# Performance work log

Hardware: AMD Instinct MI355X
Metric: run time of the kernel (lower is better)

The kernel has to match this reference:

```python
import jax, jax.numpy as jnp
import numpy as np

T, KBLK, EMB, B = 2048, 64, 512, 4


def _make_coords(t, k):
    # head1: for each j, cols = block_start(j) + arange(j % k + 1)  (block-causal local)
    j = np.arange(t)
    cnt1 = (j % k) + 1
    rows1 = np.repeat(j, cnt1)
    off1 = np.arange(cnt1.sum()) - np.repeat(np.cumsum(cnt1) - cnt1, cnt1)
    cols1 = (rows1 // k) * k + off1
    # head2: for each block start c, rows = arange(c, t), col = c  (strided block-start)
    starts = np.arange(t // k) * k
    cnt2 = t - starts
    base = np.repeat(starts, cnt2)
    off2 = np.arange(cnt2.sum()) - np.repeat(np.cumsum(cnt2) - cnt2, cnt2)
    rows2, cols2 = base + off2, base
    c1 = np.stack([rows1, cols1], 1).astype(np.int32)
    c2 = np.stack([rows2, cols2], 1).astype(np.int32)
    return c1, c2


def setup_inputs() -> dict:
    key = jax.random.key(0)
    ks = jax.random.split(key, 6)
    s = 1.0 / float(np.sqrt(EMB))
    c1, c2 = _make_coords(T, KBLK)
    return {
        "x": jax.random.normal(ks[0], (B, T, EMB), jnp.float32),
        "Wk": jax.random.normal(ks[1], (EMB, EMB), jnp.float32) * s,
        "bk": jnp.zeros((EMB,), jnp.float32),
        "Wq": jax.random.normal(ks[2], (EMB, EMB), jnp.float32) * s,
        "bq": jnp.zeros((EMB,), jnp.float32),
        "Wv": jax.random.normal(ks[3], (EMB, EMB), jnp.float32) * s,
        "bv": jnp.zeros((EMB,), jnp.float32),
        "Wu": jax.random.normal(ks[4], (EMB, 2 * EMB), jnp.float32) * s,
        "bu": jnp.zeros((EMB,), jnp.float32),
        "coords1": jnp.asarray(c1),
        "coords2": jnp.asarray(c2),
    }


def _sparse_head(Kt, Qt, Vt, coords):
    rows, cols = coords[:, 0], coords[:, 1]
    # dot[b,p] = (K @ Q^T)[b, rows[p], cols[p]] = K[b,rows[p],:] . Q[b,cols[p],:]
    dot = jnp.einsum('bpe,bpe->bp', Kt[:, rows], Qt[:, cols])
    # sparse.batchmm: out[b,r] = sum_{p: rows[p]=r} dot[b,p] * V[b, cols[p]]
    out = jnp.zeros_like(Vt).at[:, rows].add(dot[..., None] * Vt[:, cols])
    return out


def reference(x, Wk, bk, Wq, bq, Wv, bv, Wu, bu, coords1, coords2):
    Kt = x @ Wk.T + bk
    Qt = x @ Wq.T + bq
    Vt = x @ Wv.T + bv
    h1 = _sparse_head(Kt, Qt, Vt, coords1)
    h2 = _sparse_head(Kt, Qt, Vt, coords2)
    comb = jnp.concatenate([h1, h2], axis=-1)  # [B, T, 2*EMB]
    return comb @ Wu.T + bu
```

## Files before the change

kernel.cpp:

```cpp
#include <hip/hip_runtime.h>


typedef unsigned short u16;
typedef __attribute__((ext_vector_type(8))) short short8;
typedef __attribute__((ext_vector_type(4))) float f32x4;

constexpr int TDIM  = 2048;
constexpr int EMB_D = 512;
constexpr int BB    = 4;
constexpr int NBLK  = 32;
constexpr int LDK   = 2048;

__device__ __forceinline__ u16 f2b(float f) {
    unsigned u = __float_as_uint(f);
    unsigned r = (u + 0x7FFFu + ((u >> 16) & 1u)) >> 16;
    return (u16)r;
}

__global__ __launch_bounds__(256) void prep_k(
    const float* __restrict__ x, const float* __restrict__ Wk, const float* __restrict__ Wq,
    const float* __restrict__ Wv, const float* __restrict__ Wu,
    const float* __restrict__ bk, const float* __restrict__ bq, const float* __restrict__ bv,
    u16* __restrict__ xb, u16* __restrict__ wcat, u16* __restrict__ wvtb,
    u16* __restrict__ wub, float* __restrict__ biascat)
{
    const int bid = blockIdx.x, tid = threadIdx.x;
    if (bid < 5120) {
        const float* src; u16* dst; int base;
        if (bid < 4096)      { src = x;  dst = xb;            base = bid * 1024; }
        else if (bid < 4352) { src = Wk; dst = wcat;          base = (bid - 4096) * 1024; }
        else if (bid < 4608) { src = Wq; dst = wcat + 262144; base = (bid - 4352) * 1024; }
        else                 { src = Wu; dst = wub;           base = (bid - 4608) * 1024; }
        const int idx = base + tid * 4;
        float4 v = *(const float4*)(src + idx);
        ushort4 o = { f2b(v.x), f2b(v.y), f2b(v.z), f2b(v.w) };
        *(ushort4*)(dst + idx) = o;
    } else if (bid < 5184) {
        __shared__ float T[64][65];
        const int t = bid - 5120;
        const int j0 = (t >> 3) * 64, k0 = (t & 7) * 64;
        const int rr = tid >> 4, c4 = (tid & 15) * 4;
        #pragma unroll
        for (int it = 0; it < 4; ++it) {
            const int j = rr + it * 16;
            float4 v = *(const float4*)(Wv + (size_t)(j0 + j) * 512 + k0 + c4);
            T[c4+0][j] = v.x; T[c4+1][j] = v.y; T[c4+2][j] = v.z; T[c4+3][j] = v.w;
        }
        __syncthreads();
        #pragma unroll
        for (int it = 0; it < 4; ++it) {
            const int k = rr + it * 16;
            ushort4 o = { f2b(T[k][c4+0]), f2b(T[k][c4+1]), f2b(T[k][c4+2]), f2b(T[k][c4+3]) };
            *(ushort4*)(wvtb + (size_t)(k0 + k) * 512 + j0 + c4) = o;
        }
    } else if (bid < 5200) {
        const int o = (bid - 5184) * 64 + (tid >> 2);
        const int p = tid & 3;
        const int n = o & 511, half = o >> 9;
        const float* wr = Wu + (size_t)n * 1024 + half * 512 + p * 128;
        const float* br = bv + p * 128;
        float s = 0.f;
        #pragma unroll
        for (int j = 0; j < 128; j += 4) {
            float4 a = *(const float4*)(wr + j);
            float4 b = *(const float4*)(br + j);
            s += a.x*b.x + a.y*b.y + a.z*b.z + a.w*b.w;
        }
        s += __shfl_xor(s, 1);
        s += __shfl_xor(s, 2);
        if (p == 0) biascat[1024 + o] = s;
    } else {
        const int idx = tid * 4;
        float4 v = (idx < 512) ? *(const float4*)(bk + idx)
                               : *(const float4*)(bq + idx - 512);
        *(float4*)(biascat + idx) = v;
    }
}

__global__ __launch_bounds__(256) void wc_gemm_k(
    const u16* __restrict__ wub, const u16* __restrict__ wvtb, u16* __restrict__ wcat)
{
    __shared__ u16 As[128 * 32];
    __shared__ u16 Bs[128 * 32];
    const int bm = blockIdx.x * 128;
    const int bn = blockIdx.y * 128;
    const int tid  = threadIdx.x;
    const int wid  = tid >> 6;
    const int lane = tid & 63;
    const int l15  = lane & 15;
    const int quad = lane >> 4;
    const int wm = (wid & 1) * 64;
    const int wn = (wid >> 1) * 64;

    f32x4 acc[4][4] = {};

    const int srow  = tid >> 2;
    const int skoff = (tid & 3) * 8;
    const int m0 = bm + srow, m1 = bm + 64 + srow;
    const u16* Ag0 = wub + (size_t)(m0 & 511) * 1024 + (m0 >> 9) * 512 + skoff;
    const u16* Ag1 = wub + (size_t)(m1 & 511) * 1024 + (m1 >> 9) * 512 + skoff;
    const u16* Bg  = wvtb + (size_t)(bn + srow) * 512 + skoff;
    char* AsBase = (char*)As + wid * 1024;
    char* BsBase = (char*)Bs + wid * 1024;

    for (int k0 = 0; k0 < 512; k0 += 32) {
        __syncthreads();
        __builtin_amdgcn_global_load_lds(
            (const __attribute__((address_space(1))) void*)(Ag0 + k0),
            (__attribute__((address_space(3))) void*)AsBase, 16, 0, 0);
        __builtin_amdgcn_global_load_lds(
            (const __attribute__((address_space(1))) void*)(Ag1 + k0),
            (__attribute__((address_space(3))) void*)(AsBase + 4096), 16, 0, 0);
        __builtin_amdgcn_global_load_lds(
            (const __attribute__((address_space(1))) void*)(Bg + k0),
            (__attribute__((address_space(3))) void*)BsBase, 16, 0, 0);
        __builtin_amdgcn_global_load_lds(
            (const __attribute__((address_space(1))) void*)(Bg + (size_t)64 * 512 + k0),
            (__attribute__((address_space(3))) void*)(BsBase + 4096), 16, 0, 0);
        __syncthreads();

        short8 a[4], b[4];
        #pragma unroll
        for (int i = 0; i < 4; ++i)
            a[i] = *(const short8*)((const short*)As + (wm + 16 * i + l15) * 32 + quad * 8);
        #pragma unroll
        for (int j = 0; j < 4; ++j)
            b[j] = *(const short8*)((const short*)Bs + (wn + 16 * j + l15) * 32 + quad * 8);
        #pragma unroll
        for (int i = 0; i < 4; ++i)
            #pragma unroll
            for (int j = 0; j < 4; ++j)
                acc[i][j] = __builtin_amdgcn_mfma_f32_16x16x32_bf16(a[i], b[j], acc[i][j], 0, 0, 0);
    }

    #pragma unroll
    for (int i = 0; i < 4; ++i)
        #pragma unroll
        for (int j = 0; j < 4; ++j) {
            const int col = bn + wn + 16 * j + l15;
            #pragma unroll
            for (int r = 0; r < 4; ++r) {
                const int row = bm + wm + 16 * i + quad * 4 + r;
                wcat[(size_t)(1024 + row) * 512 + col] = f2b(acc[i][j][r]);
            }
        }
}

template<int MH, int KK>
__device__ __forceinline__ void mm16(const short8 (&a)[4], const short8 (&b)[2][4],
                                     f32x4 (&acc)[8][4])
{
    #pragma unroll
    for (int f = 0; f < 4; ++f)
        #pragma unroll
        for (int g = 0; g < 4; ++g)
            acc[MH * 4 + f][g] = __builtin_amdgcn_mfma_f32_16x16x32_bf16(
                a[f], b[KK][g], acc[MH * 4 + f][g], 0, 0, 0);
}

template<int SLOT, int MH>
__device__ __forceinline__ void lda4(short8 (&a)[4], const u16* sm, int arow, int koff)
{
    #pragma unroll
    for (int f = 0; f < 4; ++f)
        a[f] = *(const short8*)(sm + SLOT * 32768 + (arow + MH * 64 + f * 16) * 64 + koff);
}

template<int SLOT>
__device__ __forceinline__ void ldb4(short8 (&bk)[4], const u16* sm, int brow, int koff)
{
    #pragma unroll
    for (int g = 0; g < 4; ++g)
        bk[g] = *(const short8*)(sm + SLOT * 32768 + 16384 + (brow + g * 16) * 64 + koff);
}

#define STA(S, CI, T) __builtin_amdgcn_global_load_lds( \
    (const __attribute__((address_space(1))) void*)(Ag + (size_t)(CI) * 32768 + (T) * 64), \
    (__attribute__((address_space(3))) void*)(sm + (S) * 32768 + (CI) * 4096 + wid * 512), 16, 0, 0)
#define STB(S, CI, T) __builtin_amdgcn_global_load_lds( \
    (const __attribute__((address_space(1))) void*)(Bg + (size_t)(CI) * 32768 + (T) * 64), \
    (__attribute__((address_space(3))) void*)(sm + (S) * 32768 + 16384 + (CI) * 4096 + wid * 512), 16, 0, 0)
#define KBAR()  __builtin_amdgcn_s_barrier()
#define KPRIO(P) __builtin_amdgcn_s_setprio(P)
#define LGKM0() do { asm volatile("s_waitcnt lgkmcnt(0)" ::: "memory"); \
                     __builtin_amdgcn_sched_barrier(0); } while (0)
#define VMC4()  asm volatile("s_waitcnt vmcnt(4)" ::: "memory")
#define VMC0()  asm volatile("s_waitcnt vmcnt(0)" ::: "memory")

__global__ __launch_bounds__(512, 2) void kqv_gemm_k(
    const u16* __restrict__ A, const u16* __restrict__ W,
    const float* __restrict__ bias, u16* __restrict__ C)
{
    __shared__ u16 sm[65536];

    const int bid = blockIdx.x;
    const int wg  = (bid & 7) * 32 + (bid >> 3);
    const int bm  = (wg & 31) * 256;
    const int bn  = (wg >> 5) * 256;
    const int tid  = threadIdx.x;
    const int wid  = tid >> 6;
    const int lane = tid & 63;
    const int l15  = lane & 15;
    const int quad = lane >> 4;
    const int wm = wid >> 2;
    const int wn = wid & 3;

    const int stgrow = wid * 8 + (lane >> 3);
    const int stgk   = ((lane & 7) ^ ((lane >> 3) & 7)) << 3;
    const u16* Ag = A + (size_t)(bm + stgrow) * 512 + stgk;
    const u16* Bg = W + (size_t)(bn + stgrow) * 512 + stgk;

    const int r7     = l15 & 7;
    const int arow   = wm * 128 + l15;
    const int brow   = wn * 64 + l15;
    const int off_k0 = ((quad ^ r7) << 3);
    const int off_k1 = (((4 | quad) ^ r7) << 3);

    f32x4 acc[8][4] = {};
    short8 a[4], b[2][4];

    STA(0,0,0); STA(0,2,0); STB(0,0,0); STB(0,1,0);
    STB(0,2,0); STB(0,3,0); STA(0,1,0); STA(0,3,0);
    STA(1,0,1); STA(1,2,1); STB(1,0,1); STB(1,1,1);
    VMC4(); KBAR();

    for (int it = 0; it < 3; ++it) {
        const int t = 2 * it;
        ldb4<0>(b[0], sm, brow, off_k0); lda4<0,0>(a, sm, arow, off_k0);
        STB(1,2,t+1); STB(1,3,t+1);
        KBAR(); LGKM0(); KPRIO(1); mm16<0,0>(a, b, acc); KPRIO(0); KBAR();
        ldb4<0>(b[1], sm, brow, off_k1); lda4<0,0>(a, sm, arow, off_k1);
        STA(1,1,t+1); STA(1,3,t+1);
        KBAR(); LGKM0(); KPRIO(1); mm16<0,1>(a, b, acc); KPRIO(0); KBAR();
        lda4<0,1>(a, sm, arow, off_k0);
        STA(0,0,t+2); STA(0,2,t+2);
        KBAR(); LGKM0(); KPRIO(1); mm16<1,0>(a, b, acc); KPRIO(0); KBAR();
        lda4<0,1>(a, sm, arow, off_k1);
        STB(0,0,t+2); STB(0,1,t+2);
        KBAR(); LGKM0(); KPRIO(1); mm16<1,1>(a, b, acc); KPRIO(0); VMC4(); KBAR();
        ldb4<1>(b[0], sm, brow, off_k0); lda4<1,0>(a, sm, arow, off_k0);
        STB(0,2,t+2); STB(0,3,t+2);
        KBAR(); LGKM0(); KPRIO(1); mm16<0,0>(a, b, acc); KPRIO(0); KBAR();
        ldb4<1>(b[1], sm, brow, off_k1); lda4<1,0>(a, sm, arow, off_k1);
        STA(0,1,t+2); STA(0,3,t+2);
        KBAR(); LGKM0(); KPRIO(1); mm16<0,1>(a, b, acc); KPRIO(0); KBAR();
        lda4<1,1>(a, sm, arow, off_k0);
        STA(1,0,t+3); STA(1,2,t+3);
        KBAR(); LGKM0(); KPRIO(1); mm16<1,0>(a, b, acc); KPRIO(0); KBAR();
        lda4<1,1>(a, sm, arow, off_k1);
        STB(1,0,t+3); STB(1,1,t+3);
        KBAR(); LGKM0(); KPRIO(1); mm16<1,1>(a, b, acc); KPRIO(0); VMC4(); KBAR();
    }

    ldb4<0>(b[0], sm, brow, off_k0); lda4<0,0>(a, sm, arow, off_k0);
    STB(1,2,7); STB(1,3,7);
    KBAR(); LGKM0(); KPRIO(1); mm16<0,0>(a, b, acc); KPRIO(0); KBAR();
    ldb4<0>(b[1], sm, brow, off_k1); lda4<0,0>(a, sm, arow, off_k1);
    STA(1,1,7); STA(1,3,7);
    KBAR(); LGKM0(); KPRIO(1); mm16<0,1>(a, b, acc); KPRIO(0); KBAR();
    lda4<0,1>(a, sm, arow, off_k0);
    KBAR(); LGKM0(); KPRIO(1); mm16<1,0>(a, b, acc); KPRIO(0); KBAR();
    lda4<0,1>(a, sm, arow, off_k1);
    KBAR(); LGKM0(); KPRIO(1); mm16<1,1>(a, b, acc); KPRIO(0); VMC0(); KBAR();
    ldb4<1>(b[0], sm, brow, off_k0); lda4<1,0>(a, sm, arow, off_k0);
    KBAR(); LGKM0(); KPRIO(1); mm16<0,0>(a, b, acc); KPRIO(0); KBAR();
    ldb4<1>(b[1], sm, brow, off_k1); lda4<1,0>(a, sm, arow, off_k1);
    KBAR(); LGKM0(); KPRIO(1); mm16<0,1>(a, b, acc); KPRIO(0); KBAR();
    lda4<1,1>(a, sm, arow, off_k0);
    KBAR(); LGKM0(); KPRIO(1); mm16<1,0>(a, b, acc); KPRIO(0); KBAR();
    lda4<1,1>(a, sm, arow, off_k1);
    KBAR(); LGKM0(); KPRIO(1); mm16<1,1>(a, b, acc); KPRIO(0);

    #pragma unroll
    for (int mf = 0; mf < 8; ++mf) {
        #pragma unroll
        for (int g = 0; g < 4; ++g) {
            const int col = bn + wn * 64 + g * 16 + l15;
            const float bvv = bias[col];
            #pragma unroll
            for (int r = 0; r < 4; ++r) {
                const int row = bm + wm * 128 + mf * 16 + quad * 4 + r;
                C[(size_t)row * LDK + col] = f2b(acc[mf][g][r] + bvv);
            }
        }
    }
}

#undef STA
#undef STB
#undef KBAR
#undef KPRIO
#undef LGKM0
#undef VMC4
#undef VMC0

__global__ __launch_bounds__(256) void heads_k(
    const u16* __restrict__ KQV, const float* __restrict__ bu, float* __restrict__ out)
{
    __shared__ u16 smA[64 * 104];
    __shared__ u16 smVT[128 * 104];
    __shared__ u16 pK[2][64 * 32];
    __shared__ u16 pQ[2][64 * 32];
    __shared__ u16 pQs[2][32 * 32];

    const int blk = blockIdx.x, b = blockIdx.y;
    const int e0 = blockIdx.z * 128;
    const int tid = threadIdx.x;
    const int wid = tid >> 6, lane = tid & 63;
    const int l15 = lane & 15, quad = lane >> 4;
    const size_t row0 = (size_t)b * TDIM + (size_t)blk * 64;
    const size_t brow = (size_t)b * TDIM;
    const int srow_base = 16 * wid + quad * 4;

    #pragma unroll
    for (int it = 0; it < 4; ++it) {
        const int id = tid + 256 * it;
        const int c  = id & 63;
        const int eo = (id >> 6) * 8;
        short8 v = *(const short8*)(KQV + (row0 + c) * (size_t)LDK + 1024 + e0 + eo);
        #pragma unroll
        for (int i = 0; i < 8; ++i) smVT[(eo + i) * 104 + c] = (u16)v[i];
    }
    #pragma unroll
    for (int it = 0; it < 2; ++it) {
        const int id = tid + 256 * it;
        const int m  = id & 31;
        const int eo = (id >> 5) * 8;
        short8 v = *(const short8*)(KQV + (brow + 64 * m) * (size_t)LDK + 1536 + e0 + eo);
        #pragma unroll
        for (int i = 0; i < 8; ++i) smVT[(eo + i) * 104 + 64 + m] = (u16)v[i];
    }

    f32x4 s1[4] = {}; f32x4 s2[2] = {};
    const int srow  = tid >> 2;
    const int skoff = (tid & 3) * 8;
    const int qsrow = srow & 31;
    const int qsp   = tid >> 7;
    const u16* Kg  = KQV + (row0 + srow) * (size_t)LDK + skoff;
    const u16* Qg  = KQV + (row0 + srow) * (size_t)LDK + 512 + skoff;
    const u16* Qsg = KQV + (brow + (size_t)64 * qsrow) * (size_t)LDK + 512 + qsp * 32 + skoff;
    char* dK  = (char*)pK  + wid * 1024;
    char* dQ  = (char*)pQ  + wid * 1024;
    char* dQs = (char*)pQs + wid * 1024;

    for (int k0 = 0; k0 < 512; k0 += 64) {
        __syncthreads();
        __builtin_amdgcn_global_load_lds(
            (const __attribute__((address_space(1))) void*)(Kg + k0),
            (__attribute__((address_space(3))) void*)dK, 16, 0, 0);
        __builtin_amdgcn_global_load_lds(
            (const __attribute__((address_space(1))) void*)(Kg + k0 + 32),
            (__attribute__((address_space(3))) void*)(dK + 4096), 16, 0, 0);
        __builtin_amdgcn_global_load_lds(
            (const __attribute__((address_space(1))) void*)(Qg + k0),
            (__attribute__((address_space(3))) void*)dQ, 16, 0, 0);
        __builtin_amdgcn_global_load_lds(
            (const __attribute__((address_space(1))) void*)(Qg + k0 + 32),
            (__attribute__((address_space(3))) void*)(dQ + 4096), 16, 0, 0);
        __builtin_amdgcn_global_load_lds(
            (const __attribute__((address_space(1))) void*)(Qsg + k0),
            (__attribute__((address_space(3))) void*)dQs, 16, 0, 0);
        __syncthreads();

        short8 a0 = *(const short8*)(pK[0] + (16 * wid + l15) * 32 + quad * 8);
        short8 a1 = *(const short8*)(pK[1] + (16 * wid + l15) * 32 + quad * 8);
        #pragma unroll
        for (int j = 0; j < 4; ++j) {
            short8 b0 = *(const short8*)(pQ[0] + (16 * j + l15) * 32 + quad * 8);
            short8 b1 = *(const short8*)(pQ[1] + (16 * j + l15) * 32 + quad * 8);
            s1[j] = __builtin_amdgcn_mfma_f32_16x16x32_bf16(a0, b0, s1[j], 0, 0, 0);
            s1[j] = __builtin_amdgcn_mfma_f32_16x16x32_bf16(a1, b1, s1[j], 0, 0, 0);
        }
        #pragma unroll
        for (int j = 0; j < 2; ++j) {
            short8 b0 = *(const short8*)(pQs[0] + (16 * j + l15) * 32 + quad * 8);
            short8 b1 = *(const short8*)(pQs[1] + (16 * j + l15) * 32 + quad * 8);
            s2[j] = __builtin_amdgcn_mfma_f32_16x16x32_bf16(a0, b0, s2[j], 0, 0, 0);
            s2[j] = __builtin_amdgcn_mfma_f32_16x16x32_bf16(a1, b1, s2[j], 0, 0, 0);
        }
    }

    #pragma unroll
    for (int j = 0; j < 4; ++j)
        #pragma unroll
        for (int r = 0; r < 4; ++r) {
            const int rr = srow_base + r;
            const int cc = 16 * j + l15;
            smA[rr * 104 + cc] = f2b((cc <= rr) ? s1[j][r] : 0.0f);
        }
    #pragma unroll
    for (int j = 0; j < 2; ++j)
        #pragma unroll
        for (int r = 0; r < 4; ++r) {
            const int m  = 16 * j + l15;
            const int rr = srow_base + r;
            smA[rr * 104 + 64 + m] = f2b((m <= blk) ? s2[j][r] : 0.0f);
        }
    __syncthreads();

    f32x4 o[8] = {};
    const u16* arow = smA + (16 * wid + l15) * 104;
    #pragma unroll
    for (int ks = 0; ks < 3; ++ks) {
        short8 as = *(const short8*)(arow + 32 * ks + quad * 8);
        #pragma unroll
        for (int nt = 0; nt < 8; ++nt) {
            short8 bs = *(const short8*)(smVT + (16 * nt + l15) * 104 + 32 * ks + quad * 8);
            o[nt] = __builtin_amdgcn_mfma_f32_16x16x32_bf16(as, bs, o[nt], 0, 0, 0);
        }
    }
    #pragma unroll
    for (int nt = 0; nt < 8; ++nt) {
        const int col = e0 + 16 * nt + l15;
        const float bvv = bu[col];
        #pragma unroll
        for (int r = 0; r < 4; ++r)
            out[(row0 + srow_base + r) * (size_t)EMB_D + col] = o[nt][r] + bvv;
    }
}

extern "C" void kernel_launch(void* const* d_in, const int* in_sizes, int n_in,
                              void* d_out, int out_size, void* d_ws, size_t ws_size,
                              hipStream_t stream)
{
    const float* x  = (const float*)d_in[0];
    const float* Wk = (const float*)d_in[1];
    const float* bk = (const float*)d_in[2];
    const float* Wq = (const float*)d_in[3];
    const float* bq = (const float*)d_in[4];
    const float* Wv = (const float*)d_in[5];
    const float* bv = (const float*)d_in[6];
    const float* Wu = (const float*)d_in[7];
    const float* bu = (const float*)d_in[8];
    float* out = (float*)d_out;

    char* w = (char*)d_ws;
    u16*   KQV     = (u16*)  (w + ((size_t)0  << 20));
    u16*   xb      = (u16*)  (w + ((size_t)32 << 20));
    u16*   wcat    = (u16*)  (w + ((size_t)40 << 20));
    u16*   wvtb    = (u16*)  (w + ((size_t)42 << 20));
    u16*   wub     = (u16*)  (w + ((size_t)43 << 20));
    float* biascat = (float*)(w + ((size_t)44 << 20));

    hipLaunchKernelGGL(prep_k, dim3(5201), dim3(256), 0, stream,
                       x, Wk, Wq, Wv, Wu, bk, bq, bv, xb, wcat, wvtb, wub, biascat);
    hipLaunchKernelGGL(wc_gemm_k, dim3(8, 4), dim3(256), 0, stream, wub, wvtb, wcat);
    hipLaunchKernelGGL(kqv_gemm_k, dim3(256), dim3(512), 0, stream, xb, wcat, biascat, KQV);
    hipLaunchKernelGGL(heads_k, dim3(NBLK, BB, 4), dim3(256), 0, stream, KQV, bu, out);
}
```

Before: 144.4 us.

## Fuse Wu·Wv weight GEMM into prep kernel and stage KQV stores through LDS

The separate wc_gemm_k launch and the intermediate bf16 copies of Wu and transposed Wv are removed. The first 32 blocks of prep_k now compute the Wu·Wv product directly from fp32 global memory, converting to bf16 in registers, which saves one launch and two intermediate buffers. The Wv operand is read with strided scalar loads, and these 32 long blocks may now sit on the critical path of prep_k. Separately, the KQV GEMM epilogue writes results into shared memory first and then issues coalesced 16-byte row stores, replacing scattered 2-byte global writes.

```diff
diff --git a/kernel.cpp b/kernel.cpp
--- a/kernel.cpp
+++ b/kernel.cpp
@@ -21,40 +21,80 @@
     const float* __restrict__ x, const float* __restrict__ Wk, const float* __restrict__ Wq,
     const float* __restrict__ Wv, const float* __restrict__ Wu,
     const float* __restrict__ bk, const float* __restrict__ bq, const float* __restrict__ bv,
-    u16* __restrict__ xb, u16* __restrict__ wcat, u16* __restrict__ wvtb,
-    u16* __restrict__ wub, float* __restrict__ biascat)
+    u16* __restrict__ xb, u16* __restrict__ wcat, float* __restrict__ biascat)
 {
     const int bid = blockIdx.x, tid = threadIdx.x;
-    if (bid < 5120) {
+    if (bid < 32) {
+        const int bm = (bid >> 2) * 128;
+        const int bn = (bid & 3) * 128;
+        const int wid  = tid >> 6;
+        const int lane = tid & 63;
+        const int l15  = lane & 15;
+        const int quad = lane >> 4;
+        const int wm = (wid & 1) * 64;
+        const int wn = (wid >> 1) * 64;
+
+        f32x4 acc[4][4] = {};
+
+        const float* Arow[4];
+        #pragma unroll
+        for (int i = 0; i < 4; ++i) {
+            const int m = bm + wm + 16 * i + l15;
+            Arow[i] = Wu + (size_t)(m & 511) * 1024 + (m >> 9) * 512 + quad * 8;
+        }
+        const float* Bcol[4];
+        #pragma unroll
+        for (int g = 0; g < 4; ++g)
+            Bcol[g] = Wv + (bn + wn + 16 * g + l15) + (size_t)(quad * 8) * 512;
+
+        for (int j0 = 0; j0 < 512; j0 += 32) {
+            short8 a[4], b[4];
+            #pragma unroll
+            for (int i = 0; i < 4; ++i) {
+                float4 v0 = *(const float4*)(Arow[i] + j0);
+                float4 v1 = *(const float4*)(Arow[i] + j0 + 4);
+                a[i] = (short8){(short)f2b(v0.x), (short)f2b(v0.y), (short)f2b(v0.z), (short)f2b(v0.w),
+                                (short)f2b(v1.x), (short)f2b(v1.y), (short)f2b(v1.z), (short)f2b(v1.w)};
+            }
+            #pragma unroll
+            for (int g = 0; g < 4; ++g) {
+                const float* p = Bcol[g] + (size_t)j0 * 512;
+                float v0 = p[0];          float v1 = p[512];
+                float v2 = p[1024];       float v3 = p[1536];
+                float v4 = p[2048];       float v5 = p[2560];
+                float v6 = p[3072];       float v7 = p[3584];
+                b[g] = (short8){(short)f2b(v0), (short)f2b(v1), (short)f2b(v2), (short)f2b(v3),
+                                (short)f2b(v4), (short)f2b(v5), (short)f2b(v6), (short)f2b(v7)};
+            }
+            #pragma unroll
+            for (int i = 0; i < 4; ++i)
+                #pragma unroll
+                for (int g = 0; g < 4; ++g)
+                    acc[i][g] = __builtin_amdgcn_mfma_f32_16x16x32_bf16(a[i], b[g], acc[i][g], 0, 0, 0);
+        }
+
+        #pragma unroll
+        for (int i = 0; i < 4; ++i)
+            #pragma unroll
+            for (int g = 0; g < 4; ++g) {
+                const int col = bn + wn + 16 * g + l15;
+                #pragma unroll
+                for (int r = 0; r < 4; ++r) {
+                    const int row = bm + wm + 16 * i + quad * 4 + r;
+                    wcat[(size_t)(1024 + row) * 512 + col] = f2b(acc[i][g][r]);
+                }
+            }
+    } else if (bid < 4640) {
         const float* src; u16* dst; int base;
-        if (bid < 4096)      { src = x;  dst = xb;            base = bid * 1024; }
-        else if (bid < 4352) { src = Wk; dst = wcat;          base = (bid - 4096) * 1024; }
-        else if (bid < 4608) { src = Wq; dst = wcat + 262144; base = (bid - 4352) * 1024; }
-        else                 { src = Wu; dst = wub;           base = (bid - 4608) * 1024; }
+        if (bid < 4128)      { src = x;  dst = xb;            base = (bid - 32) * 1024; }
+        else if (bid < 4384) { src = Wk; dst = wcat;          base = (bid - 4128) * 1024; }
+        else                 { src = Wq; dst = wcat + 262144; base = (bid - 4384) * 1024; }
         const int idx = base + tid * 4;
         float4 v = *(const float4*)(src + idx);
         ushort4 o = { f2b(v.x), f2b(v.y), f2b(v.z), f2b(v.w) };
         *(ushort4*)(dst + idx) = o;
-    } else if (bid < 5184) {
-        __shared__ float T[64][65];
-        const int t = bid - 5120;
-        const int j0 = (t >> 3) * 64, k0 = (t & 7) * 64;
-        const int rr = tid >> 4, c4 = (tid & 15) * 4;
-        #pragma unroll
-        for (int it = 0; it < 4; ++it) {
-            const int j = rr + it * 16;
-            float4 v = *(const float4*)(Wv + (size_t)(j0 + j) * 512 + k0 + c4);
-            T[c4+0][j] = v.x; T[c4+1][j] = v.y; T[c4+2][j] = v.z; T[c4+3][j] = v.w;
-        }
-        __syncthreads();
-        #pragma unroll
-        for (int it = 0; it < 4; ++it) {
-            const int k = rr + it * 16;
-            ushort4 o = { f2b(T[k][c4+0]), f2b(T[k][c4+1]), f2b(T[k][c4+2]), f2b(T[k][c4+3]) };
-            *(ushort4*)(wvtb + (size_t)(k0 + k) * 512 + j0 + c4) = o;
-        }
-    } else if (bid < 5200) {
-        const int o = (bid - 5184) * 64 + (tid >> 2);
+    } else if (bid < 4656) {
+        const int o = (bid - 4640) * 64 + (tid >> 2);
         const int p = tid & 3;
         const int n = o & 511, half = o >> 9;
         const float* wr = Wu + (size_t)n * 1024 + half * 512 + p * 128;
@@ -75,75 +115,6 @@
                                : *(const float4*)(bq + idx - 512);
         *(float4*)(biascat + idx) = v;
     }
-}
-
-__global__ __launch_bounds__(256) void wc_gemm_k(
-    const u16* __restrict__ wub, const u16* __restrict__ wvtb, u16* __restrict__ wcat)
-{
-    __shared__ u16 As[128 * 32];
-    __shared__ u16 Bs[128 * 32];
-    const int bm = blockIdx.x * 128;
-    const int bn = blockIdx.y * 128;
-    const int tid  = threadIdx.x;
-    const int wid  = tid >> 6;
-    const int lane = tid & 63;
-    const int l15  = lane & 15;
-    const int quad = lane >> 4;
-    const int wm = (wid & 1) * 64;
-    const int wn = (wid >> 1) * 64;
-
-    f32x4 acc[4][4] = {};
-
-    const int srow  = tid >> 2;
-    const int skoff = (tid & 3) * 8;
-    const int m0 = bm + srow, m1 = bm + 64 + srow;
-    const u16* Ag0 = wub + (size_t)(m0 & 511) * 1024 + (m0 >> 9) * 512 + skoff;
-    const u16* Ag1 = wub + (size_t)(m1 & 511) * 1024 + (m1 >> 9) * 512 + skoff;
-    const u16* Bg  = wvtb + (size_t)(bn + srow) * 512 + skoff;
-    char* AsBase = (char*)As + wid * 1024;
-    char* BsBase = (char*)Bs + wid * 1024;
-
-    for (int k0 = 0; k0 < 512; k0 += 32) {
-        __syncthreads();
-        __builtin_amdgcn_global_load_lds(
-            (const __attribute__((address_space(1))) void*)(Ag0 + k0),
-            (__attribute__((address_space(3))) void*)AsBase, 16, 0, 0);
-        __builtin_amdgcn_global_load_lds(
-            (const __attribute__((address_space(1))) void*)(Ag1 + k0),
-            (__attribute__((address_space(3))) void*)(AsBase + 4096), 16, 0, 0);
-        __builtin_amdgcn_global_load_lds(
-            (const __attribute__((address_space(1))) void*)(Bg + k0),
-            (__attribute__((address_space(3))) void*)BsBase, 16, 0, 0);
-        __builtin_amdgcn_global_load_lds(
-            (const __attribute__((address_space(1))) void*)(Bg + (size_t)64 * 512 + k0),
-            (__attribute__((address_space(3))) void*)(BsBase + 4096), 16, 0, 0);
-        __syncthreads();
-
-        short8 a[4], b[4];
-        #pragma unroll
-        for (int i = 0; i < 4; ++i)
-            a[i] = *(const short8*)((const short*)As + (wm + 16 * i + l15) * 32 + quad * 8);
-        #pragma unroll
-        for (int j = 0; j < 4; ++j)
-            b[j] = *(const short8*)((const short*)Bs + (wn + 16 * j + l15) * 32 + quad * 8);
-        #pragma unroll
-        for (int i = 0; i < 4; ++i)
-            #pragma unroll
-            for (int j = 0; j < 4; ++j)
-                acc[i][j] = __builtin_amdgcn_mfma_f32_16x16x32_bf16(a[i], b[j], acc[i][j], 0, 0, 0);
-    }
-
-    #pragma unroll
-    for (int i = 0; i < 4; ++i)
-        #pragma unroll
-        for (int j = 0; j < 4; ++j) {
-            const int col = bn + wn + 16 * j + l15;
-            #pragma unroll
-            for (int r = 0; r < 4; ++r) {
-                const int row = bm + wm + 16 * i + quad * 4 + r;
-                wcat[(size_t)(1024 + row) * 512 + col] = f2b(acc[i][j][r]);
-            }
-        }
 }
 
 template<int MH, int KK>
@@ -271,17 +242,29 @@
     lda4<1,1>(a, sm, arow, off_k1);
     KBAR(); LGKM0(); KPRIO(1); mm16<1,1>(a, b, acc); KPRIO(0);
 
+    __syncthreads();
     #pragma unroll
     for (int mf = 0; mf < 8; ++mf) {
         #pragma unroll
         for (int g = 0; g < 4; ++g) {
-            const int col = bn + wn * 64 + g * 16 + l15;
-            const float bvv = bias[col];
+            const int col = wn * 64 + g * 16 + l15;
+            const float bvv = bias[bn + col];
             #pragma unroll
             for (int r = 0; r < 4; ++r) {
-                const int row = bm + wm * 128 + mf * 16 + quad * 4 + r;
-                C[(size_t)row * LDK + col] = f2b(acc[mf][g][r] + bvv);
+                const int row = wm * 128 + mf * 16 + quad * 4 + r;
+                sm[row * 256 + col] = f2b(acc[mf][g][r] + bvv);
             }
+        }
+    }
+    __syncthreads();
+    {
+        const int rr = tid >> 5;
+        const int ck = tid & 31;
+        #pragma unroll
+        for (int p = 0; p < 16; ++p) {
+            const int row = p * 16 + rr;
+            short8 v = *(const short8*)(sm + row * 256 + ck * 8);
+            *(short8*)(C + (size_t)(bm + row) * LDK + bn + ck * 8) = v;
         }
     }
 }
@@ -438,13 +421,10 @@
     u16*   KQV     = (u16*)  (w + ((size_t)0  << 20));
     u16*   xb      = (u16*)  (w + ((size_t)32 << 20));
     u16*   wcat    = (u16*)  (w + ((size_t)40 << 20));
-    u16*   wvtb    = (u16*)  (w + ((size_t)42 << 20));
-    u16*   wub     = (u16*)  (w + ((size_t)43 << 20));
     float* biascat = (float*)(w + ((size_t)44 << 20));
 
-    hipLaunchKernelGGL(prep_k, dim3(5201), dim3(256), 0, stream,
-                       x, Wk, Wq, Wv, Wu, bk, bq, bv, xb, wcat, wvtb, wub, biascat);
-    hipLaunchKernelGGL(wc_gemm_k, dim3(8, 4), dim3(256), 0, stream, wub, wvtb, wcat);
+    hipLaunchKernelGGL(prep_k, dim3(4657), dim3(256), 0, stream,
+                       x, Wk, Wq, Wv, Wu, bk, bq, bv, xb, wcat, biascat);
     hipLaunchKernelGGL(kqv_gemm_k, dim3(256), dim3(512), 0, stream, xb, wcat, biascat, KQV);
     hipLaunchKernelGGL(heads_k, dim3(NBLK, BB, 4), dim3(256), 0, stream, KQV, bu, out);
 }
```

New measurement: 141.6 us. About the same (-1.9%).
